# Performance work log

Measured on AMD Instinct MI355X. Metric: run time of the kernel, lower is better.

Reference implementation:

```python
import jax, jax.numpy as jnp
import numpy as np

B, A, C = 524288, 4, 9  # C = input_size + 1 (first channel is the initial hidden state)


def setup_inputs() -> dict:
    key = jax.random.key(0)
    ks = jax.random.split(key, 7)
    s = 1.0  # nn.GRU/Linear init is uniform(-1,1) for hidden=1; normal is fine for a numeric baseline
    return {
        "inputs": jax.random.normal(ks[0], (B, A, C), dtype=jnp.float32),
        "w_ih": jax.random.normal(ks[1], (3, C - 1), dtype=jnp.float32) * s,
        "w_hh": jax.random.normal(ks[2], (3, 1), dtype=jnp.float32) * s,
        "b_ih": jax.random.normal(ks[3], (3,), dtype=jnp.float32) * s,
        "b_hh": jax.random.normal(ks[4], (3,), dtype=jnp.float32) * s,
        "w_out": jax.random.normal(ks[5], (1, 1), dtype=jnp.float32) * s,
        "b_out": jax.random.normal(ks[6], (1,), dtype=jnp.float32) * s,
    }


def reference(inputs, w_ih, w_hh, b_ih, b_hh, w_out, b_out):
    b, a, c = inputs.shape
    flat = inputs.reshape(b * a, c)
    h = flat[:, :1]          # [N,1] initial hidden state
    x = flat[:, 1:]          # [N,C-1] GRU input (single timestep)
    gi = x @ w_ih.T + b_ih   # [N,3] input gates (r,z,n order, PyTorch convention)
    gh = h @ w_hh.T + b_hh   # [N,3] hidden gates
    r = jax.nn.sigmoid(gi[:, 0:1] + gh[:, 0:1])
    z = jax.nn.sigmoid(gi[:, 1:2] + gh[:, 1:2])
    n = jnp.tanh(gi[:, 2:3] + r * gh[:, 2:3])
    h_new = (1.0 - z) * n + z * h            # [N,1]
    out = h_new * w_out[0, 0] + b_out[0]     # Linear(1,1)
    return out.reshape(b, a, 1)
```

## Files before the change

kernel.cpp:

```cpp
#include <hip/hip_runtime.h>

__global__ __launch_bounds__(256) void gru_cell_kernel(
    const float* __restrict__ in,
    const float* __restrict__ w_ih,
    const float* __restrict__ w_hh,
    const float* __restrict__ b_ih,
    const float* __restrict__ b_hh,
    const float* __restrict__ w_out,
    const float* __restrict__ b_out,
    float* __restrict__ out,
    int n_rows)
{
    const int tid = blockIdx.x * blockDim.x + threadIdx.x;
    const int row0 = tid * 4;
    if (row0 >= n_rows) return;

    float wih[3][8];
#pragma unroll
    for (int g = 0; g < 3; ++g)
#pragma unroll
        for (int c = 0; c < 8; ++c)
            wih[g][c] = w_ih[g * 8 + c];
    const float whh0 = w_hh[0], whh1 = w_hh[1], whh2 = w_hh[2];
    const float bi0 = b_ih[0], bi1 = b_ih[1], bi2 = b_ih[2];
    const float bh0 = b_hh[0], bh1 = b_hh[1], bh2 = b_hh[2];
    const float wo = w_out[0], bo = b_out[0];

    float4 v[9];
    const float4* src = reinterpret_cast<const float4*>(in + (size_t)row0 * 9);
#pragma unroll
    for (int i = 0; i < 9; ++i) v[i] = src[i];
    const float* f = reinterpret_cast<const float*>(v);

    float4 o;
    float* op = reinterpret_cast<float*>(&o);
#pragma unroll
    for (int r = 0; r < 4; ++r) {
        const float* row = f + r * 9;
        const float h = row[0];
        float gi0 = bi0, gi1 = bi1, gi2 = bi2;
#pragma unroll
        for (int c = 0; c < 8; ++c) {
            const float x = row[1 + c];
            gi0 = fmaf(x, wih[0][c], gi0);
            gi1 = fmaf(x, wih[1][c], gi1);
            gi2 = fmaf(x, wih[2][c], gi2);
        }
        const float gh0 = fmaf(h, whh0, bh0);
        const float gh1 = fmaf(h, whh1, bh1);
        const float gh2 = fmaf(h, whh2, bh2);

        const float rg = 1.0f / (1.0f + __expf(-(gi0 + gh0)));
        const float z  = 1.0f / (1.0f + __expf(-(gi1 + gh1)));
        const float nn = tanhf(fmaf(rg, gh2, gi2));
        const float hn = (1.0f - z) * nn + z * h;
        op[r] = fmaf(hn, wo, bo);
    }
    *reinterpret_cast<float4*>(out + row0) = o;
}

extern "C" void kernel_launch(void* const* d_in, const int* in_sizes, int n_in,
                              void* d_out, int out_size, void* d_ws, size_t ws_size,
                              hipStream_t stream) {
    (void)n_in; (void)d_ws; (void)ws_size;
    const float* in    = (const float*)d_in[0];
    const float* w_ih  = (const float*)d_in[1];
    const float* w_hh  = (const float*)d_in[2];
    const float* b_ih  = (const float*)d_in[3];
    const float* b_hh  = (const float*)d_in[4];
    const float* w_out = (const float*)d_in[5];
    const float* b_out = (const float*)d_in[6];
    float* out = (float*)d_out;

    const int n_rows = out_size;
    const int rows_per_thread = 4;
    const int block = 256;
    const int threads = (n_rows + rows_per_thread - 1) / rows_per_thread;
    const int grid = (threads + block - 1) / block;

    gru_cell_kernel<<<grid, block, 0, stream>>>(in, w_ih, w_hh, b_ih, b_hh,
                                                w_out, b_out, out, n_rows);
}
```

Before: 18.76 us.

## Stage input through LDS for coalesced loads and use exp-based tanh

Input loads now go through shared memory. Consecutive threads read consecutive float4s, so the global loads are fully coalesced instead of each thread reading a strided 144-byte chunk. The data is scattered into a padded per-thread LDS layout (stride 37 floats) and read back after a barrier. tanhf is replaced with an exp-based formula, which cuts transcendental cost at some accuracy risk. The block also needs 37 KB of LDS and a __syncthreads, and loads for a partial tail block are unguarded (that block is only reached when the row count is not a multiple of 1024).

```diff
diff --git a/kernel.cpp b/kernel.cpp
--- a/kernel.cpp
+++ b/kernel.cpp
@@ -1,6 +1,14 @@
 #include <hip/hip_runtime.h>
 
-__global__ __launch_bounds__(256) void gru_cell_kernel(
+
+constexpr int BLOCK = 256;
+constexpr int RPT   = 4;
+constexpr int RPB   = BLOCK * RPT;
+constexpr int F4PB  = RPB * 9 / 4;
+constexpr int F4PT  = F4PB / BLOCK;
+constexpr int CHUNK_F = RPT * 9 + 1;
+
+__global__ __launch_bounds__(BLOCK) void gru_cell_kernel(
     const float* __restrict__ in,
     const float* __restrict__ w_ih,
     const float* __restrict__ w_hh,
@@ -11,9 +19,22 @@
     float* __restrict__ out,
     int n_rows)
 {
-    const int tid = blockIdx.x * blockDim.x + threadIdx.x;
-    const int row0 = tid * 4;
-    if (row0 >= n_rows) return;
+    __shared__ float lds[BLOCK * CHUNK_F];
+
+    const int t = threadIdx.x;
+    const int blk = blockIdx.x;
+    const size_t f4_base = (size_t)blk * F4PB;
+
+    const float4* src = reinterpret_cast<const float4*>(in);
+#pragma unroll
+    for (int k = 0; k < F4PT; ++k) {
+        const int j = k * BLOCK + t;
+        float4 v = src[f4_base + j];
+        const int c = j / 9;
+        const int m = j - c * 9;
+        float* dst = &lds[c * CHUNK_F + m * 4];
+        dst[0] = v.x; dst[1] = v.y; dst[2] = v.z; dst[3] = v.w;
+    }
 
     float wih[3][8];
 #pragma unroll
@@ -26,17 +47,14 @@
     const float bh0 = b_hh[0], bh1 = b_hh[1], bh2 = b_hh[2];
     const float wo = w_out[0], bo = b_out[0];
 
-    float4 v[9];
-    const float4* src = reinterpret_cast<const float4*>(in + (size_t)row0 * 9);
-#pragma unroll
-    for (int i = 0; i < 9; ++i) v[i] = src[i];
-    const float* f = reinterpret_cast<const float*>(v);
+    __syncthreads();
 
+    const float* chunk = &lds[t * CHUNK_F];
     float4 o;
     float* op = reinterpret_cast<float*>(&o);
 #pragma unroll
-    for (int r = 0; r < 4; ++r) {
-        const float* row = f + r * 9;
+    for (int r = 0; r < RPT; ++r) {
+        const float* row = chunk + r * 9;
         const float h = row[0];
         float gi0 = bi0, gi1 = bi1, gi2 = bi2;
 #pragma unroll
@@ -52,17 +70,21 @@
 
         const float rg = 1.0f / (1.0f + __expf(-(gi0 + gh0)));
         const float z  = 1.0f / (1.0f + __expf(-(gi1 + gh1)));
-        const float nn = tanhf(fmaf(rg, gh2, gi2));
+        const float y  = fmaf(rg, gh2, gi2);
+        const float nn = 2.0f / (1.0f + __expf(-2.0f * y)) - 1.0f;
         const float hn = (1.0f - z) * nn + z * h;
         op[r] = fmaf(hn, wo, bo);
     }
-    *reinterpret_cast<float4*>(out + row0) = o;
+
+    const size_t out_f4 = (size_t)blk * BLOCK + t;
+    if ((out_f4 + 1) * 4 <= (size_t)n_rows)
+        reinterpret_cast<float4*>(out)[out_f4] = o;
 }
 
 extern "C" void kernel_launch(void* const* d_in, const int* in_sizes, int n_in,
                               void* d_out, int out_size, void* d_ws, size_t ws_size,
                               hipStream_t stream) {
-    (void)n_in; (void)d_ws; (void)ws_size;
+    (void)n_in; (void)d_ws; (void)ws_size; (void)in_sizes;
     const float* in    = (const float*)d_in[0];
     const float* w_ih  = (const float*)d_in[1];
     const float* w_hh  = (const float*)d_in[2];
@@ -73,11 +95,8 @@
     float* out = (float*)d_out;
 
     const int n_rows = out_size;
-    const int rows_per_thread = 4;
-    const int block = 256;
-    const int threads = (n_rows + rows_per_thread - 1) / rows_per_thread;
-    const int grid = (threads + block - 1) / block;
+    const int grid = (n_rows + RPB - 1) / RPB;
 
-    gru_cell_kernel<<<grid, block, 0, stream>>>(in, w_ih, w_hh, b_ih, b_hh,
+    gru_cell_kernel<<<grid, BLOCK, 0, stream>>>(in, w_ih, w_hh, b_ih, b_hh,
                                                 w_out, b_out, out, n_rows);
 }
```

Result: slower. 19.26 us (+2.7%).
